# Kernel optimization log

Measured on AMD Instinct MI355X. Metric: run time of the kernel, lower is better.

The kernel has to match this reference:

```python
import jax, jax.numpy as jnp
import numpy as np

B, C_IN, C_OUT, RED, H, W = 8, 256, 64, 16, 256, 256
K = 3


def setup_inputs() -> dict:
    key = jax.random.key(0)
    k1, k2, k3, k4, k5 = jax.random.split(key, 5)
    x = jax.random.normal(k1, (B, C_OUT, H, W), dtype=jnp.float32)
    vec = jax.random.normal(k2, (B, C_IN), dtype=jnp.float32)
    # ChanNorm affine params
    g = jnp.ones((1, C_OUT, 1, 1), dtype=jnp.float32)
    b = jnp.zeros((1, C_OUT, 1, 1), dtype=jnp.float32)
    # conv_du MLP (torch Linear weights: [out, in], no bias)
    w1 = jax.random.normal(k3, (C_IN // RED, C_IN), dtype=jnp.float32) / np.sqrt(C_IN)
    w2 = jax.random.normal(k4, (C_OUT, C_IN // RED), dtype=jnp.float32) / np.sqrt(C_IN // RED)
    # Conv2DMod weight, kaiming normal fan_in (leaky_relu a=0): std=sqrt(2/fan_in)
    fan_in = C_OUT * K * K
    wconv = jax.random.normal(k5, (C_OUT, C_OUT, K, K), dtype=jnp.float32) * np.sqrt(2.0 / fan_in)
    return {"x": x, "vec": vec, "g": g, "b": b, "w1": w1, "w2": w2, "wconv": wconv}


def reference(x, vec, g, b, w1, w2, wconv):
    eps_norm = 1e-5
    eps_mod = 1e-8
    # ChanNorm: normalize over channel dim (unbiased=False var)
    mean = jnp.mean(x, axis=1, keepdims=True)
    var = jnp.mean((x - mean) ** 2, axis=1, keepdims=True)
    nx = (x - mean) / jnp.sqrt(var + eps_norm) * g + b
    # style MLP: Linear -> LeakyReLU(0.1) -> Linear (no biases)
    hid = jax.nn.leaky_relu(vec @ w1.T, negative_slope=0.1)
    sty = hid @ w2.T  # [B, C_OUT]
    # per-sample modulated weights: [B, O, I, K, K]
    weights = wconv[None, :, :, :, :] * (sty[:, None, :, None, None] + 1.0)
    # demodulate
    d = jax.lax.rsqrt(jnp.sum(weights ** 2, axis=(2, 3, 4), keepdims=True) + eps_mod)
    weights = weights * d
    # grouped conv with groups=B == per-sample conv; same padding for k=3,s=1,d=1 -> 1
    pad = ((H - 1) * 0 + 1 * (K - 1)) // 2
    def per_sample_conv(xi, wi):
        # xi: [C,H,W], wi: [O,I,K,K]
        return jax.lax.conv_general_dilated(
            xi[None], wi, window_strides=(1, 1),
            padding=[(pad, pad), (pad, pad)],
            dimension_numbers=("NCHW", "OIHW", "NCHW"))[0]
    out = jax.vmap(per_sample_conv)(nx, weights)  # [B, O, H, W]
    return out + x
```

## Files before the change

### kernel.cpp

```cpp
#include <hip/hip_runtime.h>
#include <hip/hip_bf16.h>

typedef __hip_bfloat16 bf16;
typedef __attribute__((ext_vector_type(8))) short short8;
typedef __attribute__((ext_vector_type(4))) float float4v;

#define Hd 256
#define Wd 256
#define HW 65536
#define CO 64

__global__ __launch_bounds__(64) void k1_style(
    const float* __restrict__ vec, const float* __restrict__ w1,
    const float* __restrict__ w2, const float* __restrict__ wconv,
    bf16* __restrict__ wA)
{
    int o = blockIdx.x;
    int s = blockIdx.y;
    int i = threadIdx.x;

    float sv[4];
#pragma unroll
    for (int q = 0; q < 4; ++q) sv[q] = vec[s * 256 + q * 64 + i];

    float hid[16];
#pragma unroll
    for (int j = 0; j < 16; ++j) {
        float p = 0.f;
#pragma unroll
        for (int q = 0; q < 4; ++q) p += sv[q] * w1[j * 256 + q * 64 + i];
#pragma unroll
        for (int off = 32; off >= 1; off >>= 1) p += __shfl_xor(p, off, 64);
        hid[j] = p > 0.f ? p : 0.1f * p;
    }
    float sty = 0.f;
#pragma unroll
    for (int j = 0; j < 16; ++j) sty += w2[i * 16 + j] * hid[j];
    float msty = sty + 1.0f;

    float wrow[9];
#pragma unroll
    for (int tt = 0; tt < 9; ++tt) wrow[tt] = wconv[(o * 64 + i) * 9 + tt] * msty;
    float ss = 0.f;
#pragma unroll
    for (int tt = 0; tt < 9; ++tt) ss += wrow[tt] * wrow[tt];
#pragma unroll
    for (int off = 32; off >= 1; off >>= 1) ss += __shfl_xor(ss, off, 64);
    float d = rsqrtf(ss + 1e-8f);

    bf16* wAs = wA + s * (18 * 64 * 32);
#pragma unroll
    for (int tt = 0; tt < 9; ++tt) {
        int k = tt * 64 + i;
        wAs[(k >> 5) * 2048 + o * 32 + (k & 31)] = (bf16)(wrow[tt] * d);
    }
}

#define PXB 32
#define ROWS 8
#define TR 10
#define WL 34
#define ROW_ELEMS (8 * WL * 8)

union U4 { uint4 u; bf16 h[8]; short8 s8; };

template<int WSBIG>
__global__ __launch_bounds__(256, 3) void k3_fused(
    const float* __restrict__ x, const float* __restrict__ gg,
    const float* __restrict__ bb, const bf16* __restrict__ wA,
    float* __restrict__ out)
{
    int w0 = blockIdx.x * PXB;
    int h0 = blockIdx.y * ROWS;
    int s  = blockIdx.z;
    int t  = threadIdx.x;
    __shared__ __align__(16) bf16 tile[TR * ROW_ELEMS];
    __shared__ float sg[64], sb[64];
    __shared__ float2 sbi[64];
    __shared__ float2 sms[TR * WL];
    if (t < 64) {
        float gv = gg[t];
        sg[t] = gv; sb[t] = bb[t];
        sbi[t] = make_float2(bb[t], 1.0f / gv);
    }
    __syncthreads();

    int p0 = t, p1 = t + 256;
    bool live1 = (p1 < TR * WL);
    int dr0 = p0 / WL, wl0 = p0 - dr0 * WL;
    int dr1 = live1 ? (p1 / WL) : 0;
    int wl1 = live1 ? (p1 - dr1 * WL) : 0;
    int grow0 = h0 + dr0 - 1, wab0 = w0 + wl0 - 1;
    int grow1 = h0 + dr1 - 1, wab1 = w0 + wl1 - 1;
    bool ok0 = (grow0 >= 0 && grow0 < Hd && wab0 >= 0 && wab0 < Wd);
    bool ok1 = live1 && (grow1 >= 0 && grow1 < Hd && wab1 >= 0 && wab1 < Wd);
    const float* xp0 = x + (size_t)s * (CO * HW) + (size_t)grow0 * Wd + wab0;
    const float* xp1 = x + (size_t)s * (CO * HW) + (size_t)grow1 * Wd + wab1;
    bf16* dst0 = &tile[dr0 * ROW_ELEMS + wl0 * 8];
    bf16* dst1 = &tile[dr1 * ROW_ELEMS + wl1 * 8];

    float s1a = 0.f, s2a = 0.f, s1b = 0.f, s2b = 0.f;
#pragma unroll 1
    for (int c8 = 0; c8 < 8; ++c8) {
        U4 pa, pb;
        if (ok0) {
#pragma unroll
            for (int k = 0; k < 8; ++k) {
                float f = xp0[(size_t)(c8 * 8 + k) * HW];
                s1a += f; s2a += f * f;
                pa.h[k] = (bf16)f;
            }
        } else pa.u = make_uint4(0u, 0u, 0u, 0u);
        *(uint4*)&dst0[c8 * (WL * 8)] = pa.u;
        if (live1) {
            if (ok1) {
#pragma unroll
                for (int k = 0; k < 8; ++k) {
                    float f = xp1[(size_t)(c8 * 8 + k) * HW];
                    s1b += f; s2b += f * f;
                    pb.h[k] = (bf16)f;
                }
            } else pb.u = make_uint4(0u, 0u, 0u, 0u);
            *(uint4*)&dst1[c8 * (WL * 8)] = pb.u;
        }
    }

    {
        float mean = s1a * (1.f / 64);
        float var  = s2a * (1.f / 64) - mean * mean;
        float rstd = rsqrtf(var + 1e-5f);
        sms[p0] = ok0 ? make_float2(mean, sqrtf(var + 1e-5f)) : make_float2(0.f, 0.f);
        if (ok0) {
#pragma unroll 1
            for (int c8 = 0; c8 < 8; ++c8) {
                U4 v; v.u = *(uint4*)&dst0[c8 * (WL * 8)];
                U4 o;
#pragma unroll
                for (int k = 0; k < 8; ++k) {
                    int c = c8 * 8 + k;
                    o.h[k] = (bf16)((__bfloat162float(v.h[k]) - mean) * rstd * sg[c] + sb[c]);
                }
                *(uint4*)&dst0[c8 * (WL * 8)] = o.u;
            }
        }
    }
    if (live1) {
        float mean = s1b * (1.f / 64);
        float var  = s2b * (1.f / 64) - mean * mean;
        float rstd = rsqrtf(var + 1e-5f);
        sms[p1] = ok1 ? make_float2(mean, sqrtf(var + 1e-5f)) : make_float2(0.f, 0.f);
        if (ok1) {
#pragma unroll 1
            for (int c8 = 0; c8 < 8; ++c8) {
                U4 v; v.u = *(uint4*)&dst1[c8 * (WL * 8)];
                U4 o;
#pragma unroll
                for (int k = 0; k < 8; ++k) {
                    int c = c8 * 8 + k;
                    o.h[k] = (bf16)((__bfloat162float(v.h[k]) - mean) * rstd * sg[c] + sb[c]);
                }
                *(uint4*)&dst1[c8 * (WL * 8)] = o.u;
            }
        }
    }
    __syncthreads();

    int wave = t >> 6, lane = t & 63;
    int mi = wave & 1, ni = wave >> 1;
    int col = lane & 15, quad = lane >> 4;
    const bf16* wAs = wA + s * (18 * 64 * 32);

    float4v acc[2][ROWS];
#pragma unroll
    for (int mt = 0; mt < 2; ++mt)
#pragma unroll
        for (int r = 0; r < ROWS; ++r) acc[mt][r] = (float4v)0.f;

#pragma unroll 1
    for (int kh = 0; kh < 3; ++kh) {
#pragma unroll
        for (int kw = 0; kw < 3; ++kw) {
#pragma unroll
            for (int half = 0; half < 2; ++half) {
                int kc = (kh * 3 + kw) * 2 + half;
                U4 a0, a1;
                a0.u = *(const uint4*)&wAs[kc * 2048 + (mi * 32 + col) * 32 + quad * 8];
                a1.u = *(const uint4*)&wAs[kc * 2048 + (mi * 32 + 16 + col) * 32 + quad * 8];
                int ch8 = half * 4 + quad;
                const bf16* bbase = &tile[kh * ROW_ELEMS + (ch8 * WL + ni * 16 + col + kw) * 8];
#pragma unroll
                for (int r = 0; r < ROWS; ++r) {
                    U4 b; b.u = *(const uint4*)&bbase[r * ROW_ELEMS];
                    acc[0][r] = __builtin_amdgcn_mfma_f32_16x16x32_bf16(a0.s8, b.s8, acc[0][r], 0, 0, 0);
                    acc[1][r] = __builtin_amdgcn_mfma_f32_16x16x32_bf16(a1.s8, b.s8, acc[1][r], 0, 0, 0);
                }
            }
        }
    }

    int wpx  = w0 + ni * 16 + col;
    int wl_i = ni * 16 + col + 1;
#pragma unroll
    for (int r = 0; r < ROWS; ++r) {
        int grow = h0 + r;
        float2 ms = sms[(r + 1) * WL + wl_i];
#pragma unroll
        for (int mt = 0; mt < 2; ++mt) {
#pragma unroll
            for (int rr = 0; rr < 4; ++rr) {
                int o = mi * 32 + mt * 16 + quad * 4 + rr;
                float nxf = __bfloat162float(
                    tile[(r + 1) * ROW_ELEMS + ((o >> 3) * WL + wl_i) * 8 + (o & 7)]);
                float2 bi = sbi[o];
                float xrec = (nxf - bi.x) * bi.y * ms.y + ms.x;
                size_t idx = (size_t)(s * CO + o) * HW + (size_t)grow * Wd + wpx;
                out[idx] = acc[mt][r][rr] + xrec;
            }
        }
    }
}

extern "C" void kernel_launch(void* const* d_in, const int* in_sizes, int n_in,
                              void* d_out, int out_size, void* d_ws, size_t ws_size,
                              hipStream_t stream)
{
    const float* x     = (const float*)d_in[0];
    const float* vec   = (const float*)d_in[1];
    const float* g     = (const float*)d_in[2];
    const float* bb    = (const float*)d_in[3];
    const float* w1    = (const float*)d_in[4];
    const float* w2    = (const float*)d_in[5];
    const float* wconv = (const float*)d_in[6];
    float* out = (float*)d_out;

    bf16* wA = (bf16*)d_ws;

    k1_style<<<dim3(64, 8), 64, 0, stream>>>(vec, w1, w2, wconv, wA);

    if (ws_size >= ((size_t)72 << 20))
        k3_fused<1><<<dim3(8, 32, 8), 256, 0, stream>>>(x, g, bb, wA, out);
    else
        k3_fused<0><<<dim3(8, 32, 8), 256, 0, stream>>>(x, g, bb, wA, out);
}
```

Before: 328.2 us.

## Preload weight fragments into registers and restructure normalization and MFMA loop order

```diff
diff --git a/kernel.cpp b/kernel.cpp
--- a/kernel.cpp
+++ b/kernel.cpp
@@ -60,12 +60,12 @@
 #define ROWS 8
 #define TR 10
 #define WL 34
+#define NSITES (TR * WL)
 #define ROW_ELEMS (8 * WL * 8)
 
 union U4 { uint4 u; bf16 h[8]; short8 s8; };
 
-template<int WSBIG>
-__global__ __launch_bounds__(256, 3) void k3_fused(
+__device__ __forceinline__ void k3_body(
     const float* __restrict__ x, const float* __restrict__ gg,
     const float* __restrict__ bb, const bf16* __restrict__ wA,
     float* __restrict__ out)
@@ -77,16 +77,15 @@
     __shared__ __align__(16) bf16 tile[TR * ROW_ELEMS];
     __shared__ float sg[64], sb[64];
     __shared__ float2 sbi[64];
-    __shared__ float2 sms[TR * WL];
+    __shared__ float4 sms[NSITES];
     if (t < 64) {
         float gv = gg[t];
         sg[t] = gv; sb[t] = bb[t];
         sbi[t] = make_float2(bb[t], 1.0f / gv);
     }
-    __syncthreads();
 
     int p0 = t, p1 = t + 256;
-    bool live1 = (p1 < TR * WL);
+    bool live1 = (p1 < NSITES);
     int dr0 = p0 / WL, wl0 = p0 - dr0 * WL;
     int dr1 = live1 ? (p1 / WL) : 0;
     int wl1 = live1 ? (p1 - dr1 * WL) : 0;
@@ -124,86 +123,76 @@
             *(uint4*)&dst1[c8 * (WL * 8)] = pb.u;
         }
     }
-
     {
         float mean = s1a * (1.f / 64);
         float var  = s2a * (1.f / 64) - mean * mean;
-        float rstd = rsqrtf(var + 1e-5f);
-        sms[p0] = ok0 ? make_float2(mean, sqrtf(var + 1e-5f)) : make_float2(0.f, 0.f);
-        if (ok0) {
-#pragma unroll 1
-            for (int c8 = 0; c8 < 8; ++c8) {
-                U4 v; v.u = *(uint4*)&dst0[c8 * (WL * 8)];
-                U4 o;
-#pragma unroll
-                for (int k = 0; k < 8; ++k) {
-                    int c = c8 * 8 + k;
-                    o.h[k] = (bf16)((__bfloat162float(v.h[k]) - mean) * rstd * sg[c] + sb[c]);
-                }
-                *(uint4*)&dst0[c8 * (WL * 8)] = o.u;
-            }
-        }
+        sms[p0] = ok0 ? make_float4(mean, rsqrtf(var + 1e-5f), 1.f, sqrtf(var + 1e-5f))
+                      : make_float4(0.f, 0.f, 0.f, 0.f);
     }
     if (live1) {
         float mean = s1b * (1.f / 64);
         float var  = s2b * (1.f / 64) - mean * mean;
-        float rstd = rsqrtf(var + 1e-5f);
-        sms[p1] = ok1 ? make_float2(mean, sqrtf(var + 1e-5f)) : make_float2(0.f, 0.f);
-        if (ok1) {
-#pragma unroll 1
-            for (int c8 = 0; c8 < 8; ++c8) {
-                U4 v; v.u = *(uint4*)&dst1[c8 * (WL * 8)];
-                U4 o;
-#pragma unroll
-                for (int k = 0; k < 8; ++k) {
-                    int c = c8 * 8 + k;
-                    o.h[k] = (bf16)((__bfloat162float(v.h[k]) - mean) * rstd * sg[c] + sb[c]);
-                }
-                *(uint4*)&dst1[c8 * (WL * 8)] = o.u;
-            }
-        }
+        sms[p1] = ok1 ? make_float4(mean, rsqrtf(var + 1e-5f), 1.f, sqrtf(var + 1e-5f))
+                      : make_float4(0.f, 0.f, 0.f, 0.f);
     }
     __syncthreads();
 
     int wave = t >> 6, lane = t & 63;
     int mi = wave & 1, ni = wave >> 1;
     int col = lane & 15, quad = lane >> 4;
+
     const bf16* wAs = wA + s * (18 * 64 * 32);
-
-    float4v acc[2][ROWS];
-#pragma unroll
-    for (int mt = 0; mt < 2; ++mt)
-#pragma unroll
-        for (int r = 0; r < ROWS; ++r) acc[mt][r] = (float4v)0.f;
-
+    short8 afrag[18][2];
+#pragma unroll
+    for (int kc = 0; kc < 18; ++kc)
+#pragma unroll
+        for (int mt = 0; mt < 2; ++mt) {
+            U4 a;
+            a.u = *(const uint4*)&wAs[kc * 2048 + (mi * 32 + mt * 16 + col) * 32 + quad * 8];
+            afrag[kc][mt] = a.s8;
+        }
+
+    {
+        int c8s = t >> 5, l32 = t & 31;
+        float g8[8], b8[8];
+#pragma unroll
+        for (int k = 0; k < 8; ++k) { g8[k] = sg[c8s * 8 + k]; b8[k] = sb[c8s * 8 + k]; }
 #pragma unroll 1
-    for (int kh = 0; kh < 3; ++kh) {
-#pragma unroll
-        for (int kw = 0; kw < 3; ++kw) {
-#pragma unroll
-            for (int half = 0; half < 2; ++half) {
-                int kc = (kh * 3 + kw) * 2 + half;
-                U4 a0, a1;
-                a0.u = *(const uint4*)&wAs[kc * 2048 + (mi * 32 + col) * 32 + quad * 8];
-                a1.u = *(const uint4*)&wAs[kc * 2048 + (mi * 32 + 16 + col) * 32 + quad * 8];
-                int ch8 = half * 4 + quad;
-                const bf16* bbase = &tile[kh * ROW_ELEMS + (ch8 * WL + ni * 16 + col + kw) * 8];
-#pragma unroll
-                for (int r = 0; r < ROWS; ++r) {
-                    U4 b; b.u = *(const uint4*)&bbase[r * ROW_ELEMS];
-                    acc[0][r] = __builtin_amdgcn_mfma_f32_16x16x32_bf16(a0.s8, b.s8, acc[0][r], 0, 0, 0);
-                    acc[1][r] = __builtin_amdgcn_mfma_f32_16x16x32_bf16(a1.s8, b.s8, acc[1][r], 0, 0, 0);
-                }
+        for (int e = l32; e < NSITES; e += 32) {
+            int dr = e / WL, wl = e - dr * WL;
+            float4 ms = sms[e];
+            bf16* pp = &tile[dr * ROW_ELEMS + (c8s * WL + wl) * 8];
+            U4 v; v.u = *(uint4*)pp;
+            U4 ov;
+#pragma unroll
+            for (int k = 0; k < 8; ++k) {
+                float f = __bfloat162float(v.h[k]);
+                ov.h[k] = (bf16)(((f - ms.x) * ms.y * g8[k] + b8[k]) * ms.z);
             }
-        }
-    }
-
-    int wpx  = w0 + ni * 16 + col;
-    int wl_i = ni * 16 + col + 1;
-#pragma unroll
+            *(uint4*)pp = ov.u;
+        }
+    }
+    __syncthreads();
+
+#pragma unroll 2
     for (int r = 0; r < ROWS; ++r) {
+        float4v acc[2];
+        acc[0] = (float4v)0.f; acc[1] = (float4v)0.f;
+#pragma unroll
+        for (int kc = 0; kc < 18; ++kc) {
+            int tap = kc >> 1;
+            int kh = tap / 3, kw = tap - kh * 3;
+            int ch8 = (kc & 1) * 4 + quad;
+            int wl = ni * 16 + col + kw;
+            U4 b;
+            b.u = *(const uint4*)&tile[(r + kh) * ROW_ELEMS + (ch8 * WL + wl) * 8];
+            acc[0] = __builtin_amdgcn_mfma_f32_16x16x32_bf16(afrag[kc][0], b.s8, acc[0], 0, 0, 0);
+            acc[1] = __builtin_amdgcn_mfma_f32_16x16x32_bf16(afrag[kc][1], b.s8, acc[1], 0, 0, 0);
+        }
         int grow = h0 + r;
-        float2 ms = sms[(r + 1) * WL + wl_i];
+        int wpx  = w0 + ni * 16 + col;
+        int wl_i = ni * 16 + col + 1;
+        float4 ms = sms[(r + 1) * WL + wl_i];
 #pragma unroll
         for (int mt = 0; mt < 2; ++mt) {
 #pragma unroll
@@ -212,13 +201,23 @@
                 float nxf = __bfloat162float(
                     tile[(r + 1) * ROW_ELEMS + ((o >> 3) * WL + wl_i) * 8 + (o & 7)]);
                 float2 bi = sbi[o];
-                float xrec = (nxf - bi.x) * bi.y * ms.y + ms.x;
+                float xrec = (nxf - bi.x) * bi.y * ms.w + ms.x;
                 size_t idx = (size_t)(s * CO + o) * HW + (size_t)grow * Wd + wpx;
-                out[idx] = acc[mt][r][rr] + xrec;
+                out[idx] = acc[mt][rr] + xrec;
             }
         }
     }
 }
+
+__global__ __launch_bounds__(256) void k3_fused_big(
+    const float* __restrict__ x, const float* __restrict__ gg,
+    const float* __restrict__ bb, const bf16* __restrict__ wA,
+    float* __restrict__ out) { k3_body(x, gg, bb, wA, out); }
+
+__global__ __launch_bounds__(256) void k3_fused_small(
+    const float* __restrict__ x, const float* __restrict__ gg,
+    const float* __restrict__ bb, const bf16* __restrict__ wA,
+    float* __restrict__ out) { k3_body(x, gg, bb, wA, out); }
 
 extern "C" void kernel_launch(void* const* d_in, const int* in_sizes, int n_in,
                               void* d_out, int out_size, void* d_ws, size_t ws_size,
@@ -237,8 +236,8 @@
 
     k1_style<<<dim3(64, 8), 64, 0, stream>>>(vec, w1, w2, wconv, wA);
 
-    if (ws_size >= ((size_t)72 << 20))
-        k3_fused<1><<<dim3(8, 32, 8), 256, 0, stream>>>(x, g, bb, wA, out);
+    if (ws_size >= ((size_t)80 << 20))
+        k3_fused_big<<<dim3(8, 32, 8), 256, 0, stream>>>(x, g, bb, wA, out);
     else
-        k3_fused<0><<<dim3(8, 32, 8), 256, 0, stream>>>(x, g, bb, wA, out);
+        k3_fused_small<<<dim3(8, 32, 8), 256, 0, stream>>>(x, g, bb, wA, out);
 }
```

New measurement: 314.5 us. 4.2% less time.
